# Kernel tuning notes

Hardware: AMD Instinct MI355X
Metric: run time of the kernel (lower is better)

The kernel has to match this reference:

```python
import jax, jax.numpy as jnp
import numpy as np

EMBED_DIM = 512
NUM_HEADS = 16
TGT_LEN = 1024
BSZ = 4
HEAD_DIM = EMBED_DIM // NUM_HEADS


def setup_inputs() -> dict:
    key = jax.random.key(0)
    ks = jax.random.split(key, 12)
    E = EMBED_DIM
    s = 1.0 / np.sqrt(E)
    query = jax.random.normal(ks[0], (TGT_LEN, BSZ, E), dtype=jnp.float32)
    attn_bias = jax.random.normal(ks[1], (BSZ * NUM_HEADS, TGT_LEN, TGT_LEN), dtype=jnp.float32)
    key_padding_mask = jax.random.randint(ks[2], (BSZ, TGT_LEN), 0, 2) == 1
    q_w = jax.random.normal(ks[3], (E, E), dtype=jnp.float32) * s
    q_b = jax.random.normal(ks[4], (E,), dtype=jnp.float32) * 0.02
    k_w = jax.random.normal(ks[5], (E, E), dtype=jnp.float32) * s
    k_b = jax.random.normal(ks[6], (E,), dtype=jnp.float32) * 0.02
    v_w = jax.random.normal(ks[7], (E, E), dtype=jnp.float32) * s
    v_b = jax.random.normal(ks[8], (E,), dtype=jnp.float32) * 0.02
    out_w = jax.random.normal(ks[9], (E, E), dtype=jnp.float32) * s
    out_b = jax.random.normal(ks[10], (E,), dtype=jnp.float32) * 0.02
    return {
        "query": query, "attn_bias": attn_bias, "key_padding_mask": key_padding_mask,
        "q_w": q_w, "q_b": q_b, "k_w": k_w, "k_b": k_b,
        "v_w": v_w, "v_b": v_b, "out_w": out_w, "out_b": out_b,
    }


def reference(query, attn_bias, key_padding_mask, q_w, q_b, k_w, k_b, v_w, v_b, out_w, out_b):
    Tlen, B, E = query.shape
    H, hd = NUM_HEADS, HEAD_DIM
    scaling = hd ** -0.5
    # self-attention: q/k/v all from query (Linear uses y = x @ W.T + b)
    q = (query @ q_w.T + q_b) * scaling
    k = query @ k_w.T + k_b
    v = query @ v_w.T + v_b
    # [T, B, E] -> [B*H, T, hd]
    q = q.reshape(Tlen, B * H, hd).transpose(1, 0, 2)
    k = k.reshape(Tlen, B * H, hd).transpose(1, 0, 2)
    v = v.reshape(Tlen, B * H, hd).transpose(1, 0, 2)
    # scores [B*H, T, S]
    aw = jnp.einsum('bth,bsh->bts', q, k) + attn_bias
    # key padding mask: [B, S] -> broadcast over heads and tgt
    aw = aw.reshape(B, H, Tlen, Tlen)
    aw = jnp.where(key_padding_mask[:, None, None, :], -jnp.inf, aw)
    aw = aw.reshape(B * H, Tlen, Tlen)
    probs = jax.nn.softmax(aw.astype(jnp.float32), axis=-1)
    attn = jnp.einsum('bts,bsh->bth', probs.astype(query.dtype), v)
    attn = attn.transpose(1, 0, 2).reshape(Tlen, B, E)
    out = attn @ out_w.T + out_b
    # need_weights=True, need_head_weights=False -> mean over heads, [B, T, S]
    attn_weights_avg = probs.reshape(B, H, Tlen, Tlen).mean(axis=1)
    return out, attn_weights_avg
```

## Files before the change

kernel.cpp:

```cpp
#include <hip/hip_runtime.h>
#include <math.h>

typedef __bf16 bf16x8 __attribute__((ext_vector_type(8)));
typedef __bf16 bf16x4 __attribute__((ext_vector_type(4)));
typedef float  f32x4  __attribute__((ext_vector_type(4)));

#define WAIT_LGKM0() __builtin_amdgcn_s_waitcnt(0xC07F)

__global__ __launch_bounds__(256)
void cvt_w(const float* __restrict__ w0, const float* __restrict__ w1,
           const float* __restrict__ w2, const float* __restrict__ w3,
           __bf16* __restrict__ d0, __bf16* __restrict__ d1,
           __bf16* __restrict__ d2, __bf16* __restrict__ d3)
{
    const int y = blockIdx.y;
    const float* s = (y == 0) ? w0 : (y == 1) ? w1 : (y == 2) ? w2 : w3;
    __bf16*      d = (y == 0) ? d0 : (y == 1) ? d1 : (y == 2) ? d2 : d3;
    const int i = blockIdx.x * 256 + threadIdx.x;
    float4 a = *(const float4*)(s + (size_t)i * 8);
    float4 b = *(const float4*)(s + (size_t)i * 8 + 4);
    bf16x8 v;
    v[0] = (__bf16)a.x; v[1] = (__bf16)a.y; v[2] = (__bf16)a.z; v[3] = (__bf16)a.w;
    v[4] = (__bf16)b.x; v[5] = (__bf16)b.y; v[6] = (__bf16)b.z; v[7] = (__bf16)b.w;
    *(bf16x8*)(d + (size_t)i * 8) = v;
}

__global__ __launch_bounds__(256)
void qkv_proj(const float* __restrict__ X,
              const __bf16* __restrict__ Wqb, const __bf16* __restrict__ Wkb,
              const __bf16* __restrict__ Wvb,
              const float* __restrict__ bq, const float* __restrict__ bk,
              const float* __restrict__ bv,
              __bf16* __restrict__ qTb, __bf16* __restrict__ kTb,
              __bf16* __restrict__ vTb)
{
    const int z = blockIdx.z;
    const __bf16* Wb   = (z == 0) ? Wqb : (z == 1) ? Wkb : Wvb;
    const float*  bias = (z == 0) ? bq  : (z == 1) ? bk  : bv;

    const int tid  = threadIdx.x;
    const int w    = tid >> 6;
    const int lane = tid & 63;
    const int lq   = lane & 15;
    const int quad = lane >> 4;
    const int n0    = blockIdx.x * 64 + (w >> 1) * 32;
    const int obase = blockIdx.y * 128 + (w & 1) * 64;

    f32x4 acc[2][4] = {};
#pragma unroll 2
    for (int k0 = 0; k0 < 512; k0 += 32) {
        bf16x8 af[2], bfr[4];
#pragma unroll
        for (int m = 0; m < 2; m++) {
            const float* xp = X + (size_t)(n0 + m * 16 + lq) * 512 + k0 + quad * 8;
            float4 x0 = *(const float4*)xp;
            float4 x1 = *(const float4*)(xp + 4);
            bf16x8 v;
            v[0] = (__bf16)x0.x; v[1] = (__bf16)x0.y; v[2] = (__bf16)x0.z; v[3] = (__bf16)x0.w;
            v[4] = (__bf16)x1.x; v[5] = (__bf16)x1.y; v[6] = (__bf16)x1.z; v[7] = (__bf16)x1.w;
            af[m] = v;
        }
#pragma unroll
        for (int nn = 0; nn < 4; nn++)
            bfr[nn] = *(const bf16x8*)(Wb + (size_t)(obase + nn * 16 + lq) * 512 + k0 + quad * 8);
#pragma unroll
        for (int m = 0; m < 2; m++)
#pragma unroll
            for (int nn = 0; nn < 4; nn++)
                acc[m][nn] = __builtin_amdgcn_mfma_f32_16x16x32_bf16(af[m], bfr[nn], acc[m][nn], 0, 0, 0);
    }

    const float scaling = 0.17677669529663687f;
#pragma unroll
    for (int m = 0; m < 2; m++)
#pragma unroll
        for (int nn = 0; nn < 4; nn++)
#pragma unroll
            for (int r = 0; r < 4; r++) {
                const int n = n0 + m * 16 + quad * 4 + r;
                const int o = obase + nn * 16 + lq;
                float val = acc[m][nn][r] + bias[o];
                const int t = n >> 2, b = n & 3;
                const int h = o >> 5, d = o & 31;
                const int bh = b * 16 + h;
                if (z == 0)
                    qTb[(((size_t)bh * 1024 + t) << 5) + d] = (__bf16)(val * scaling);
                else if (z == 1)
                    kTb[(((size_t)bh * 1024 + t) << 5) + d] = (__bf16)val;
                else
                    vTb[(((size_t)bh * 32 + d) << 10) + t] = (__bf16)val;
            }
}

__global__ __launch_bounds__(256)
void out_proj(const __bf16* __restrict__ A, const __bf16* __restrict__ Wb,
              const float* __restrict__ bias, float* __restrict__ out)
{
    const int tid  = threadIdx.x;
    const int w    = tid >> 6;
    const int lane = tid & 63;
    const int lq   = lane & 15;
    const int quad = lane >> 4;
    const int n0    = blockIdx.x * 64 + (w >> 1) * 32;
    const int obase = blockIdx.y * 128 + (w & 1) * 64;

    f32x4 acc[2][4] = {};
#pragma unroll 2
    for (int k0 = 0; k0 < 512; k0 += 32) {
        bf16x8 af[2], bfr[4];
#pragma unroll
        for (int m = 0; m < 2; m++)
            af[m] = *(const bf16x8*)(A + (size_t)(n0 + m * 16 + lq) * 512 + k0 + quad * 8);
#pragma unroll
        for (int nn = 0; nn < 4; nn++)
            bfr[nn] = *(const bf16x8*)(Wb + (size_t)(obase + nn * 16 + lq) * 512 + k0 + quad * 8);
#pragma unroll
        for (int m = 0; m < 2; m++)
#pragma unroll
            for (int nn = 0; nn < 4; nn++)
                acc[m][nn] = __builtin_amdgcn_mfma_f32_16x16x32_bf16(af[m], bfr[nn], acc[m][nn], 0, 0, 0);
    }
#pragma unroll
    for (int m = 0; m < 2; m++)
#pragma unroll
        for (int nn = 0; nn < 4; nn++)
#pragma unroll
            for (int r = 0; r < 4; r++) {
                const int n = n0 + m * 16 + quad * 4 + r;
                const int o = obase + nn * 16 + lq;
                out[(size_t)n * 512 + o] = acc[m][nn][r] + bias[o];
            }
}

__global__ __launch_bounds__(512, 2)
void attn_mfma(const __bf16* __restrict__ qTb, const __bf16* __restrict__ kTb,
               const __bf16* __restrict__ vTb, const float* __restrict__ bias,
               const int* __restrict__ mask, __bf16* __restrict__ attnb,
               float* __restrict__ avgf, __bf16* __restrict__ p1)
{
    __shared__ float smem[17408];
    float* const Op0  = smem;
    float* const red0 = &smem[8448];
    __bf16* const Pbase = (__bf16*)&smem[8704];

    const int tid  = threadIdx.x;
    const int w    = tid >> 6;
    const int lane = tid & 63;
    const int lq   = lane & 15;
    const int quad = lane >> 4;

    const int bid = blockIdx.y * 64 + blockIdx.x;
    const int nb  = (bid & 7) * 32 + (bid >> 3);
    const int t0  = (nb & 63) * 16;
    const int b   = nb >> 6;
    const int z   = blockIdx.z;
    const int sbase = w * 128;

    __bf16* const Pw = Pbase + w * 2176;

    unsigned mbits = 0;
    {
        const int* mp = mask + b * 1024 + sbase + quad * 4;
#pragma unroll
        for (int j = 0; j < 8; j++) {
            int4 m4 = *(const int4*)(mp + j * 16);
            mbits |= (unsigned)(m4.x != 0) << (j * 4 + 0);
            mbits |= (unsigned)(m4.y != 0) << (j * 4 + 1);
            mbits |= (unsigned)(m4.z != 0) << (j * 4 + 2);
            mbits |= (unsigned)(m4.w != 0) << (j * 4 + 3);
        }
    }

    const float* const bb = bias + (((size_t)(b * 16 + z * 8)) << 20) +
                            (((size_t)(t0 + lq)) << 10) + sbase + quad * 4;
    const __bf16* const qp0 = qTb + (((size_t)((b * 16 + z * 8) * 1024 + t0)) << 5) +
                              lq * 32 + quad * 8;
    const __bf16* const kp0 = kTb + ((size_t)(b * 16 + z * 8) << 15);
    const __bf16* const vp0 = vTb + ((size_t)(b * 16 + z * 8) << 15);

    bf16x8 qa = *(const bf16x8*)qp0;
    f32x4 cj[8];
#pragma unroll
    for (int j = 0; j < 8; j++) cj[j] = *(const f32x4*)(bb + j * 16);

    float avg_reg[32] = {};

    for (int hh = 0; hh < 8; hh++) {
        float* const Op  = Op0  + (hh & 1) * 4224;
        float* const red = red0 + (hh & 1) * 128;
        const __bf16* kp = kp0 + ((size_t)hh << 15);
        const __bf16* vp = vp0 + ((size_t)hh << 15);

        bf16x8 kb[8];
#pragma unroll
        for (int j = 0; j < 8; j++)
            kb[j] = *(const bf16x8*)(kp + (size_t)(sbase + j * 16 + lq) * 32 + quad * 8);
        bf16x8 v0r[4], v1r[4];
#pragma unroll
        for (int ks = 0; ks < 4; ks++) {
            v0r[ks] = *(const bf16x8*)(vp + (size_t)lq * 1024 + sbase + ks * 32 + quad * 8);
            v1r[ks] = *(const bf16x8*)(vp + (size_t)(16 + lq) * 1024 + sbase + ks * 32 + quad * 8);
        }
        __builtin_amdgcn_sched_barrier(0);

        f32x4 acc[8];
        __builtin_amdgcn_s_setprio(1);
#pragma unroll
        for (int j = 0; j < 8; j++)
            acc[j] = __builtin_amdgcn_mfma_f32_16x16x32_bf16(kb[j], qa, cj[j], 0, 0, 0);
        __builtin_amdgcn_s_setprio(0);
        __builtin_amdgcn_sched_barrier(0);

        {
            const int hn = (hh + 1) & 7;
            qa = *(const bf16x8*)(qp0 + ((size_t)hn << 15));
            const float* bn = bb + ((size_t)hn << 20);
#pragma unroll
            for (int j = 0; j < 8; j++) cj[j] = *(const f32x4*)(bn + j * 16);
        }
        __builtin_amdgcn_sched_barrier(0);

        float sm = 0.f;
#pragma unroll
        for (int j = 0; j < 8; j++)
#pragma unroll
            for (int r = 0; r < 4; r++) {
                float p = __expf(acc[j][r]);
                p = ((mbits >> (j * 4 + r)) & 1u) ? 0.f : p;
                acc[j][r] = p;
                sm += p;
            }
        sm += __shfl_xor(sm, 16);
        sm += __shfl_xor(sm, 32);

#pragma unroll
        for (int j = 0; j < 8; j++) {
            bf16x4 pv;
            pv[0] = (__bf16)acc[j][0]; pv[1] = (__bf16)acc[j][1];
            pv[2] = (__bf16)acc[j][2]; pv[3] = (__bf16)acc[j][3];
            *(bf16x4*)&Pw[lq * 136 + j * 16 + quad * 4] = pv;
        }
        if (lane < 16) red[w * 16 + lane] = sm;

        f32x4 o0 = {0.f, 0.f, 0.f, 0.f}, o1 = {0.f, 0.f, 0.f, 0.f};
        __builtin_amdgcn_s_setprio(1);
#pragma unroll
        for (int ks = 0; ks < 4; ks++) {
            bf16x8 pa = *(const bf16x8*)&Pw[lq * 136 + ks * 32 + quad * 8];
            o0 = __builtin_amdgcn_mfma_f32_16x16x32_bf16(pa, v0r[ks], o0, 0, 0, 0);
            o1 = __builtin_amdgcn_mfma_f32_16x16x32_bf16(pa, v1r[ks], o1, 0, 0, 0);
        }
        __builtin_amdgcn_s_setprio(0);
#pragma unroll
        for (int r = 0; r < 4; r++) {
            Op[w * 528 + (quad * 4 + r) * 33 + lq]      = o0[r];
            Op[w * 528 + (quad * 4 + r) * 33 + 16 + lq] = o1[r];
        }

        __builtin_amdgcn_sched_barrier(0);
        asm volatile("" ::: "memory");
        WAIT_LGKM0();
        __builtin_amdgcn_s_barrier();
        asm volatile("" ::: "memory");
        __builtin_amdgcn_sched_barrier(0);

        {
            const int t = tid >> 5, d = tid & 31;
            float s = 0.f, o = 0.f;
#pragma unroll
            for (int w2 = 0; w2 < 8; w2++) s += red[w2 * 16 + t];
#pragma unroll
            for (int w2 = 0; w2 < 8; w2++) o += Op[w2 * 528 + t * 33 + d];
            attnb[((size_t)(t0 + t) * 4 + b) * 512 + (z * 8 + hh) * 32 + d] =
                (__bf16)(o / s);
        }

        float s_all = 0.f;
#pragma unroll
        for (int w2 = 0; w2 < 8; w2++) s_all += red[w2 * 16 + lq];
        const float inv = 1.0f / s_all;
#pragma unroll
        for (int j = 0; j < 8; j++)
#pragma unroll
            for (int r = 0; r < 4; r++)
                avg_reg[j * 4 + r] += acc[j][r] * inv;
    }

    if (z == 0) {
        float* ap = avgf + ((size_t)(b * 1024 + t0 + lq) << 10) + sbase + quad * 4;
#pragma unroll
        for (int j = 0; j < 8; j++) {
            f32x4 v = { avg_reg[j * 4 + 0] * 0.0625f, avg_reg[j * 4 + 1] * 0.0625f,
                        avg_reg[j * 4 + 2] * 0.0625f, avg_reg[j * 4 + 3] * 0.0625f };
            *(f32x4*)(ap + j * 16) = v;
        }
    } else {
        __bf16* pp = p1 + ((size_t)(b * 1024 + t0 + lq) << 10) + sbase + quad * 4;
#pragma unroll
        for (int j = 0; j < 8; j++) {
            bf16x4 v;
            v[0] = (__bf16)(avg_reg[j * 4 + 0] * 0.0625f);
            v[1] = (__bf16)(avg_reg[j * 4 + 1] * 0.0625f);
            v[2] = (__bf16)(avg_reg[j * 4 + 2] * 0.0625f);
            v[3] = (__bf16)(avg_reg[j * 4 + 3] * 0.0625f);
            *(bf16x4*)(pp + j * 16) = v;
        }
    }
}

__global__ __launch_bounds__(256)
void avg_add(float* __restrict__ avg, const __bf16* __restrict__ p1)
{
    const size_t i = ((size_t)blockIdx.x * 256 + threadIdx.x) * 8;
    bf16x8 a = *(const bf16x8*)(p1 + i);
    float4 lo = *(float4*)(avg + i);
    float4 hi = *(float4*)(avg + i + 4);
    lo.x += (float)a[0]; lo.y += (float)a[1];
    lo.z += (float)a[2]; lo.w += (float)a[3];
    hi.x += (float)a[4]; hi.y += (float)a[5];
    hi.z += (float)a[6]; hi.w += (float)a[7];
    *(float4*)(avg + i)     = lo;
    *(float4*)(avg + i + 4) = hi;
}

extern "C" void kernel_launch(void* const* d_in, const int* in_sizes, int n_in,
                              void* d_out, int out_size, void* d_ws, size_t ws_size,
                              hipStream_t stream)
{
    const float* query     = (const float*)d_in[0];
    const float* attn_bias = (const float*)d_in[1];
    const int*   mask      = (const int*)d_in[2];
    const float* q_w       = (const float*)d_in[3];
    const float* q_b       = (const float*)d_in[4];
    const float* k_w       = (const float*)d_in[5];
    const float* k_b       = (const float*)d_in[6];
    const float* v_w       = (const float*)d_in[7];
    const float* v_b       = (const float*)d_in[8];
    const float* out_w     = (const float*)d_in[9];
    const float* out_b     = (const float*)d_in[10];

    float* out     = (float*)d_out;
    float* avg_out = out + (size_t)2097152;

    char* wsb = (char*)d_ws;
    __bf16* Wqb   = (__bf16*)(wsb);
    __bf16* Wkb   = (__bf16*)(wsb + ((size_t)512 << 10));
    __bf16* Wvb   = (__bf16*)(wsb + ((size_t)1 << 20));
    __bf16* Wob   = (__bf16*)(wsb + ((size_t)1 << 20) + ((size_t)512 << 10));
    __bf16* qTb   = (__bf16*)(wsb + ((size_t)2  << 20));
    __bf16* kTb   = (__bf16*)(wsb + ((size_t)6  << 20));
    __bf16* vTb   = (__bf16*)(wsb + ((size_t)10 << 20));
    __bf16* attnb = (__bf16*)(wsb + ((size_t)14 << 20));
    __bf16* p1    = (__bf16*)(wsb + ((size_t)18 << 20));

    cvt_w<<<dim3(128, 4), dim3(256), 0, stream>>>(
        q_w, k_w, v_w, out_w, Wqb, Wkb, Wvb, Wob);

    qkv_proj<<<dim3(64, 4, 3), dim3(256), 0, stream>>>(
        query, Wqb, Wkb, Wvb, q_b, k_b, v_b, qTb, kTb, vTb);

    attn_mfma<<<dim3(64, 4, 2), dim3(512), 0, stream>>>(
        qTb, kTb, vTb, attn_bias, mask, attnb, avg_out, p1);

    avg_add<<<dim3(2048), dim3(256), 0, stream>>>(avg_out, p1);

    out_proj<<<dim3(64, 4), dim3(256), 0, stream>>>(attnb, Wob, out_b, out);
}
```

Baseline: 171.4 us.

## Process two query sub-tiles per block to reuse K/V registers across tiles

Each attention block now covers 32 query rows, as two 16-row sub-tiles, instead of 16. The K and V fragments loaded for each head are reused for both sub-tiles, which halves K/V global loads, and the grid shrinks from 512 to 256 blocks. The block-index swizzle is redone to cover the new grid. The loop is fully unrolled and there are two sets of head-average accumulators, which raises register pressure and may hurt occupancy. It also leaves fewer blocks to hide latency.

```diff
diff --git a/kernel.cpp b/kernel.cpp
--- a/kernel.cpp
+++ b/kernel.cpp
@@ -149,11 +149,11 @@
     const int lq   = lane & 15;
     const int quad = lane >> 4;
 
-    const int bid = blockIdx.y * 64 + blockIdx.x;
-    const int nb  = (bid & 7) * 32 + (bid >> 3);
-    const int t0  = (nb & 63) * 16;
-    const int b   = nb >> 6;
-    const int z   = blockIdx.z;
+    const int bid = blockIdx.z * 128 + blockIdx.y * 32 + blockIdx.x;
+    const int swz = (bid & 7) * 32 + (bid >> 3);
+    const int t0  = (swz & 31) * 32;
+    const int b   = (swz >> 5) & 3;
+    const int z   = swz >> 7;
     const int sbase = w * 128;
 
     __bf16* const Pw = Pbase + w * 2176;
@@ -183,23 +183,28 @@
 #pragma unroll
     for (int j = 0; j < 8; j++) cj[j] = *(const f32x4*)(bb + j * 16);
 
-    float avg_reg[32] = {};
-
-    for (int hh = 0; hh < 8; hh++) {
-        float* const Op  = Op0  + (hh & 1) * 4224;
-        float* const red = red0 + (hh & 1) * 128;
-        const __bf16* kp = kp0 + ((size_t)hh << 15);
-        const __bf16* vp = vp0 + ((size_t)hh << 15);
-
-        bf16x8 kb[8];
-#pragma unroll
-        for (int j = 0; j < 8; j++)
-            kb[j] = *(const bf16x8*)(kp + (size_t)(sbase + j * 16 + lq) * 32 + quad * 8);
-        bf16x8 v0r[4], v1r[4];
-#pragma unroll
-        for (int ks = 0; ks < 4; ks++) {
-            v0r[ks] = *(const bf16x8*)(vp + (size_t)lq * 1024 + sbase + ks * 32 + quad * 8);
-            v1r[ks] = *(const bf16x8*)(vp + (size_t)(16 + lq) * 1024 + sbase + ks * 32 + quad * 8);
+    float avg_reg[2][32] = {};
+    bf16x8 kb[8];
+    bf16x8 v0r[4], v1r[4];
+
+#pragma unroll
+    for (int i = 0; i < 16; i++) {
+        const int hh = i >> 1;
+        const int ts = i & 1;
+        float* const Op  = Op0  + (i & 1) * 4224;
+        float* const red = red0 + (i & 1) * 128;
+
+        if (ts == 0) {
+            const __bf16* kp = kp0 + ((size_t)hh << 15);
+            const __bf16* vp = vp0 + ((size_t)hh << 15);
+#pragma unroll
+            for (int j = 0; j < 8; j++)
+                kb[j] = *(const bf16x8*)(kp + (size_t)(sbase + j * 16 + lq) * 32 + quad * 8);
+#pragma unroll
+            for (int ks = 0; ks < 4; ks++) {
+                v0r[ks] = *(const bf16x8*)(vp + (size_t)lq * 1024 + sbase + ks * 32 + quad * 8);
+                v1r[ks] = *(const bf16x8*)(vp + (size_t)(16 + lq) * 1024 + sbase + ks * 32 + quad * 8);
+            }
         }
         __builtin_amdgcn_sched_barrier(0);
 
@@ -212,9 +217,11 @@
         __builtin_amdgcn_sched_barrier(0);
 
         {
-            const int hn = (hh + 1) & 7;
-            qa = *(const bf16x8*)(qp0 + ((size_t)hn << 15));
-            const float* bn = bb + ((size_t)hn << 20);
+            const int in  = (i + 1) & 15;
+            const int hn  = in >> 1;
+            const int tsn = in & 1;
+            qa = *(const bf16x8*)(qp0 + ((size_t)hn << 15) + (tsn << 9));
+            const float* bn = bb + ((size_t)hn << 20) + (tsn << 14);
 #pragma unroll
             for (int j = 0; j < 8; j++) cj[j] = *(const f32x4*)(bn + j * 16);
         }
@@ -271,7 +278,7 @@
             for (int w2 = 0; w2 < 8; w2++) s += red[w2 * 16 + t];
 #pragma unroll
             for (int w2 = 0; w2 < 8; w2++) o += Op[w2 * 528 + t * 33 + d];
-            attnb[((size_t)(t0 + t) * 4 + b) * 512 + (z * 8 + hh) * 32 + d] =
+            attnb[((size_t)(t0 + ts * 16 + t) * 4 + b) * 512 + (z * 8 + hh) * 32 + d] =
                 (__bf16)(o / s);
         }
 
@@ -283,27 +290,34 @@
         for (int j = 0; j < 8; j++)
 #pragma unroll
             for (int r = 0; r < 4; r++)
-                avg_reg[j * 4 + r] += acc[j][r] * inv;
-    }
-
-    if (z == 0) {
-        float* ap = avgf + ((size_t)(b * 1024 + t0 + lq) << 10) + sbase + quad * 4;
-#pragma unroll
-        for (int j = 0; j < 8; j++) {
-            f32x4 v = { avg_reg[j * 4 + 0] * 0.0625f, avg_reg[j * 4 + 1] * 0.0625f,
-                        avg_reg[j * 4 + 2] * 0.0625f, avg_reg[j * 4 + 3] * 0.0625f };
-            *(f32x4*)(ap + j * 16) = v;
-        }
-    } else {
-        __bf16* pp = p1 + ((size_t)(b * 1024 + t0 + lq) << 10) + sbase + quad * 4;
-#pragma unroll
-        for (int j = 0; j < 8; j++) {
-            bf16x4 v;
-            v[0] = (__bf16)(avg_reg[j * 4 + 0] * 0.0625f);
-            v[1] = (__bf16)(avg_reg[j * 4 + 1] * 0.0625f);
-            v[2] = (__bf16)(avg_reg[j * 4 + 2] * 0.0625f);
-            v[3] = (__bf16)(avg_reg[j * 4 + 3] * 0.0625f);
-            *(bf16x4*)(pp + j * 16) = v;
+                avg_reg[ts][j * 4 + r] += acc[j][r] * inv;
+    }
+
+#pragma unroll
+    for (int ts = 0; ts < 2; ts++) {
+        const size_t rowbase = ((size_t)(b * 1024 + t0 + ts * 16 + lq) << 10) +
+                               sbase + quad * 4;
+        if (z == 0) {
+            float* ap = avgf + rowbase;
+#pragma unroll
+            for (int j = 0; j < 8; j++) {
+                f32x4 v = { avg_reg[ts][j * 4 + 0] * 0.0625f,
+                            avg_reg[ts][j * 4 + 1] * 0.0625f,
+                            avg_reg[ts][j * 4 + 2] * 0.0625f,
+                            avg_reg[ts][j * 4 + 3] * 0.0625f };
+                *(f32x4*)(ap + j * 16) = v;
+            }
+        } else {
+            __bf16* pp = p1 + rowbase;
+#pragma unroll
+            for (int j = 0; j < 8; j++) {
+                bf16x4 v;
+                v[0] = (__bf16)(avg_reg[ts][j * 4 + 0] * 0.0625f);
+                v[1] = (__bf16)(avg_reg[ts][j * 4 + 1] * 0.0625f);
+                v[2] = (__bf16)(avg_reg[ts][j * 4 + 2] * 0.0625f);
+                v[3] = (__bf16)(avg_reg[ts][j * 4 + 3] * 0.0625f);
+                *(bf16x4*)(pp + j * 16) = v;
+            }
         }
     }
 }
@@ -359,7 +373,7 @@
     qkv_proj<<<dim3(64, 4, 3), dim3(256), 0, stream>>>(
         query, Wqb, Wkb, Wvb, q_b, k_b, v_b, qTb, kTb, vTb);
 
-    attn_mfma<<<dim3(64, 4, 2), dim3(512), 0, stream>>>(
+    attn_mfma<<<dim3(32, 4, 2), dim3(512), 0, stream>>>(
         qTb, kTb, vTb, attn_bias, mask, attnb, avg_out, p1);
 
     avg_add<<<dim3(2048), dim3(256), 0, stream>>>(avg_out, p1);
```

After: 312.7 us. 82.4% more time.
